# Kernel tuning notes

Measured on AMD Instinct MI355X. Metric: run time of the kernel, lower is better.

The kernel has to match this reference:

```python
import jax, jax.numpy as jnp
import numpy as np

N = 100000
E = 1600000
D_IN = 128
HEADS = 4
C = 16  # hidden // heads
NEG_SLOPE = 0.2


def setup_inputs() -> dict:
    key = jax.random.key(0)
    ks = jax.random.split(key, 8)
    x = jax.random.normal(ks[0], (N, D_IN), dtype=jnp.float32)
    edge_index = jax.random.randint(ks[1], (2, E), 0, N, dtype=jnp.int32)
    s = 1.0 / np.sqrt(D_IN)
    W_l = jax.random.normal(ks[2], (D_IN, HEADS * C), dtype=jnp.float32) * s
    b_l = jnp.zeros((HEADS * C,), dtype=jnp.float32)
    W_r = jax.random.normal(ks[3], (D_IN, HEADS * C), dtype=jnp.float32) * s
    b_r = jnp.zeros((HEADS * C,), dtype=jnp.float32)
    att = jax.random.normal(ks[4], (HEADS, C), dtype=jnp.float32) * (1.0 / np.sqrt(C))
    bias = jnp.zeros((HEADS * C,), dtype=jnp.float32)
    W_head = jax.random.normal(ks[5], (HEADS * C, 1), dtype=jnp.float32) * (1.0 / np.sqrt(HEADS * C))
    b_head = jnp.zeros((1,), dtype=jnp.float32)
    return {"x": x, "edge_index": edge_index, "W_l": W_l, "b_l": b_l,
            "W_r": W_r, "b_r": b_r, "att": att, "bias": bias,
            "W_head": W_head, "b_head": b_head}


def reference(x, edge_index, W_l, b_l, W_r, b_r, att, bias, W_head, b_head):
    # GATv2Conv (PyG semantics, add_self_loops=True, concat=True)
    n = x.shape[0]
    # add self loops
    loops = jnp.arange(n, dtype=edge_index.dtype)
    src = jnp.concatenate([edge_index[0], loops])  # source j
    dst = jnp.concatenate([edge_index[1], loops])  # target i
    # per-node linear projections -> [N, H, C]
    x_l = (x @ W_l + b_l).reshape(n, HEADS, C)
    x_r = (x @ W_r + b_r).reshape(n, HEADS, C)
    # per-edge attention logits: att . LeakyReLU(x_l[j] + x_r[i])
    e = x_l[src] + x_r[dst]                               # [E', H, C]
    e = jnp.where(e >= 0, e, NEG_SLOPE * e)
    logits = jnp.einsum('ehc,hc->eh', e, att)             # [E', H]
    # segment softmax over incoming edges of each target node
    seg_max = jax.ops.segment_max(logits, dst, num_segments=n)  # [N, H]
    expw = jnp.exp(logits - seg_max[dst])
    seg_sum = jax.ops.segment_sum(expw, dst, num_segments=n)
    alpha = expw / seg_sum[dst]                           # [E', H]
    # weighted scatter-aggregate of source messages
    msg = alpha[:, :, None] * x_l[src]                    # [E', H, C]
    out = jax.ops.segment_sum(msg, dst, num_segments=n)   # [N, H, C]
    out = out.reshape(n, HEADS * C) + bias
    # ReLU + Linear head
    h = jax.nn.relu(out)
    return (h @ W_head + b_head).squeeze(-1)              # [N]
```

## Files before the change

### kernel.cpp

```cpp
#include <hip/hip_runtime.h>
#include <hip/hip_bf16.h>
#include <hip/hip_fp16.h>

#define HC 64
#define D_IN 128
#define NEG_SLOPE 0.2f
#define BK 64
#define BCAP2 1536
#define NBIN 2048
#define L2E 1.44269504f

using f32x4 = __attribute__((ext_vector_type(4))) float;
using f16x8 = __attribute__((ext_vector_type(8))) _Float16;
using f16x2 = __attribute__((ext_vector_type(2))) _Float16;

__global__ __launch_bounds__(256, 4) void k_proj(
    const float* __restrict__ x,
    const float* __restrict__ Wl, const float* __restrict__ bl,
    const float* __restrict__ Wr, const float* __restrict__ br,
    __half* __restrict__ xlh, float* __restrict__ xr,
    int* __restrict__ bfill, int N) {
    if (blockIdx.x < 8) {
        const int i = blockIdx.x * 256 + threadIdx.x;
        bfill[i] = i * BCAP2;
    }
    const int t = threadIdx.x;
    const int lane = t & 63;
    const int wave = t >> 6;
    const int m = lane & 15;
    const int q = lane >> 4;

    f16x8 bf[2][4];
    float bfu[2];
#pragma unroll
    for (int cc = 0; cc < 2; ++cc) {
        const int ct = wave * 2 + cc;
        const int ch = (ct & 3) * 16 + m;
        const float* W = (ct < 4) ? Wl : Wr;
        bfu[cc] = (ct < 4) ? bl[ch] : br[ch];
#pragma unroll
        for (int kk = 0; kk < 4; ++kk) {
            const float* wp = W + (size_t)(kk * 32 + q * 8) * 64 + ch;
            f16x8 v;
#pragma unroll
            for (int e = 0; e < 8; ++e)
                v[e] = (_Float16)wp[(size_t)e * 64];
            bf[cc][kk] = v;
        }
    }

    const int ntrip = N >> 5;
    for (int trip = blockIdx.x; trip < ntrip; trip += gridDim.x) {
        const int i0 = trip << 5;
        f16x8 af[2][4];
#pragma unroll
        for (int tt = 0; tt < 2; ++tt) {
            const float* xp = x + (size_t)(i0 + tt * 16 + m) * D_IN + q * 8;
#pragma unroll
            for (int kk = 0; kk < 4; ++kk) {
                const float4 f0 = *(const float4*)(xp + kk * 32);
                const float4 f1 = *(const float4*)(xp + kk * 32 + 4);
                f16x8 v;
                v[0] = (_Float16)f0.x; v[1] = (_Float16)f0.y;
                v[2] = (_Float16)f0.z; v[3] = (_Float16)f0.w;
                v[4] = (_Float16)f1.x; v[5] = (_Float16)f1.y;
                v[6] = (_Float16)f1.z; v[7] = (_Float16)f1.w;
                af[tt][kk] = v;
            }
        }
#pragma unroll
        for (int cc = 0; cc < 2; ++cc) {
            const int ct = wave * 2 + cc;
            f32x4 acc0 = {0.f, 0.f, 0.f, 0.f};
            f32x4 acc1 = {0.f, 0.f, 0.f, 0.f};
#pragma unroll
            for (int kk = 0; kk < 4; ++kk) {
                acc0 = __builtin_amdgcn_mfma_f32_16x16x32_f16(af[0][kk], bf[cc][kk], acc0, 0, 0, 0);
                acc1 = __builtin_amdgcn_mfma_f32_16x16x32_f16(af[1][kk], bf[cc][kk], acc1, 0, 0, 0);
            }
            const float bv = bfu[cc];
            if (ct < 4) {
                const int ch = ct * 16 + m;
#pragma unroll
                for (int r = 0; r < 4; ++r) {
                    xlh[(size_t)(i0 + q * 4 + r) * HC + ch]      = __float2half(acc0[r] + bv);
                    xlh[(size_t)(i0 + 16 + q * 4 + r) * HC + ch] = __float2half(acc1[r] + bv);
                }
            } else {
                const int ch = (ct - 4) * 16 + m;
#pragma unroll
                for (int r = 0; r < 4; ++r) {
                    xr[(size_t)(i0 + q * 4 + r) * HC + ch]      = acc0[r] + bv;
                    xr[(size_t)(i0 + 16 + q * 4 + r) * HC + ch] = acc1[r] + bv;
                }
            }
        }
    }
}

__global__ __launch_bounds__(256) void k_scat1(const int* __restrict__ src,
                                               const int* __restrict__ dst, int E,
                                               int* __restrict__ bfill,
                                               unsigned* __restrict__ coarse) {
    __shared__ int h[NBIN], bl[NBIN], cur[NBIN];
    const int t = threadIdx.x;
    for (int i = t; i < NBIN; i += 256) { h[i] = 0; cur[i] = 0; }
    __syncthreads();
    const int beg = blockIdx.x * 4096;
    int4 d4[4], s4[4];
#pragma unroll
    for (int r = 0; r < 4; ++r) {
        const int idx = beg + 4 * t + r * 1024;
        if (idx < E) {
            d4[r] = *(const int4*)(dst + idx);
            s4[r] = *(const int4*)(src + idx);
        } else { d4[r] = make_int4(-1, -1, -1, -1); }
    }
#pragma unroll
    for (int r = 0; r < 4; ++r) {
        if (d4[r].x >= 0) {
            atomicAdd(&h[d4[r].x >> 6], 1);
            atomicAdd(&h[d4[r].y >> 6], 1);
            atomicAdd(&h[d4[r].z >> 6], 1);
            atomicAdd(&h[d4[r].w >> 6], 1);
        }
    }
    __syncthreads();
    for (int i = t; i < NBIN; i += 256)
        bl[i] = h[i] ? atomicAdd(&bfill[i], h[i]) : 0;
    __syncthreads();
#pragma unroll
    for (int r = 0; r < 4; ++r) {
        if (d4[r].x >= 0) {
            const int dd[4] = {d4[r].x, d4[r].y, d4[r].z, d4[r].w};
            const int ss[4] = {s4[r].x, s4[r].y, s4[r].z, s4[r].w};
#pragma unroll
            for (int j = 0; j < 4; ++j) {
                const int bin = dd[j] >> 6;
                const int pos = atomicAdd(&cur[bin], 1);
                coarse[bl[bin] + pos] = ((unsigned)ss[j] << 6) | (unsigned)(dd[j] & 63);
            }
        }
    }
}

__device__ __forceinline__ float redpair(float v) {
    int a = __builtin_amdgcn_update_dpp(0, __float_as_int(v), 0xB1, 0xF, 0xF, true);
    return v + __int_as_float(a);
}

__global__ __launch_bounds__(256) void k_aggs(
    const __half* __restrict__ xlh, const float* __restrict__ xr,
    const float* __restrict__ att, const float* __restrict__ bias,
    const float* __restrict__ Wh, const float* __restrict__ bh,
    const int* __restrict__ bfill, const unsigned* __restrict__ coarse,
    float* __restrict__ out, int N) {
    __shared__ int s_src[BCAP2];
    __shared__ int s_cnt[BK], s_off[BK], s_cur[BK], s_scan[BK];
    const int t = threadIdx.x;
    const int b = blockIdx.x;
    const int eb = b * BCAP2;
    const int ee = bfill[b];
    if (t < BK) { s_cnt[t] = 0; s_cur[t] = 0; }
    __syncthreads();
    unsigned er[6]; int nr = 0;
#pragma unroll
    for (int r = 0; r < 6; ++r) {
        const int idx = eb + t + r * 256;
        if (idx < ee) er[nr++] = coarse[idx];
    }
    for (int k = 0; k < nr; ++k) atomicAdd(&s_cnt[er[k] & 63], 1);
    __syncthreads();
    if (t < BK) s_scan[t] = s_cnt[t];
    __syncthreads();
    for (int o = 1; o < BK; o <<= 1) {
        int v = (t < BK && t >= o) ? s_scan[t - o] : 0;
        __syncthreads();
        if (t < BK) s_scan[t] += v;
        __syncthreads();
    }
    if (t < BK) s_off[t] = s_scan[t] - s_cnt[t];
    __syncthreads();
    for (int k = 0; k < nr; ++k) {
        const int bin = er[k] & 63;
        const int pos = atomicAdd(&s_cur[bin], 1);
        s_src[s_off[bin] + pos] = (int)(er[k] >> 6);
    }
    __syncthreads();

    const int wave = t >> 6;
    const int lane = t & 63;
    const int sub  = lane & 7;
    const int slot = lane >> 3;
    const _Float16* xlhp = (const _Float16*)xlh;

    const float4 atA = *(const float4*)(att + 8 * sub);
    const float4 atB = *(const float4*)(att + 8 * sub + 4);
    f16x2 at[4];
    at[0][0] = (_Float16)(atA.x * L2E); at[0][1] = (_Float16)(atA.y * L2E);
    at[1][0] = (_Float16)(atA.z * L2E); at[1][1] = (_Float16)(atA.w * L2E);
    at[2][0] = (_Float16)(atB.x * L2E); at[2][1] = (_Float16)(atB.y * L2E);
    at[3][0] = (_Float16)(atB.z * L2E); at[3][1] = (_Float16)(atB.w * L2E);
    const f16x2 c02 = {(_Float16)NEG_SLOPE, (_Float16)NEG_SLOPE};
    const float4 biA = *(const float4*)(bias + 8 * sub);
    const float4 biB = *(const float4*)(bias + 8 * sub + 4);
    const float4 whA = *(const float4*)(Wh + 8 * sub);
    const float4 whB = *(const float4*)(Wh + 8 * sub + 4);
    const float bhv = bh[0];

    for (int k16 = 0; k16 < 16; ++k16) {
        const int nl = wave + 4 * k16;
        const int i = (b << 6) + nl;
        if (i >= N) continue;
        const int beg = s_off[nl];
        const int cnt = s_cnt[nl];

        const float4 xrA = *(const float4*)(xr + ((size_t)i << 6) + 8 * sub);
        const float4 xrB = *(const float4*)(xr + ((size_t)i << 6) + 8 * sub + 4);
        f16x2 xri[4];
        xri[0][0] = (_Float16)xrA.x; xri[0][1] = (_Float16)xrA.y;
        xri[1][0] = (_Float16)xrA.z; xri[1][1] = (_Float16)xrA.w;
        xri[2][0] = (_Float16)xrB.x; xri[2][1] = (_Float16)xrB.y;
        xri[3][0] = (_Float16)xrB.z; xri[3][1] = (_Float16)xrB.w;
        const uint4 xliraw = *(const uint4*)(xlhp + ((size_t)i << 6) + 8 * sub);
        f16x2 xli[4];
        xli[0] = __builtin_bit_cast(f16x2, xliraw.x);
        xli[1] = __builtin_bit_cast(f16x2, xliraw.y);
        xli[2] = __builtin_bit_cast(f16x2, xliraw.z);
        xli[3] = __builtin_bit_cast(f16x2, xliraw.w);

        float t0 = 0.f;
#pragma unroll
        for (int c = 0; c < 4; ++c) {
            f16x2 w = xli[c] + xri[c];
            w = __builtin_elementwise_max(w, w * c02);
            t0 = __builtin_amdgcn_fdot2(at[c], w, t0, false);
        }
        t0 = redpair(t0);
        const float pe0 = (slot == 0) ? exp2f(t0) : 0.f;
        float s = pe0;
        float a[8];
#pragma unroll
        for (int c = 0; c < 4; ++c) {
            a[2 * c]     = pe0 * (float)xli[c][0];
            a[2 * c + 1] = pe0 * (float)xli[c][1];
        }

        int p = 0;
#define EDGE_GROUP(JEXPR, PRED)                                              \
    {                                                                        \
        const int jj = (JEXPR);                                              \
        const uint4 raw = *(const uint4*)(xlhp + ((size_t)jj << 6) + 8 * sub);\
        f16x2 xv[4];                                                         \
        xv[0] = __builtin_bit_cast(f16x2, raw.x);                            \
        xv[1] = __builtin_bit_cast(f16x2, raw.y);                            \
        xv[2] = __builtin_bit_cast(f16x2, raw.z);                            \
        xv[3] = __builtin_bit_cast(f16x2, raw.w);                            \
        float tt = 0.f;                                                      \
        _Pragma("unroll")                                                    \
        for (int c = 0; c < 4; ++c) {                                        \
            f16x2 w = xv[c] + xri[c];                                        \
            w = __builtin_elementwise_max(w, w * c02);                       \
            tt = __builtin_amdgcn_fdot2(at[c], w, tt, false);                \
        }                                                                    \
        tt = redpair(tt);                                                    \
        const float pe = (PRED) ? exp2f(tt) : 0.f;                           \
        s += pe;                                                             \
        _Pragma("unroll")                                                    \
        for (int c = 0; c < 4; ++c) {                                        \
            a[2 * c]     = fmaf(pe, (float)xv[c][0], a[2 * c]);              \
            a[2 * c + 1] = fmaf(pe, (float)xv[c][1], a[2 * c + 1]);          \
        }                                                                    \
    }
        for (; p + 16 <= cnt; p += 16) {
            const int j0 = s_src[beg + p + slot];
            const int j1 = s_src[beg + p + 8 + slot];
            EDGE_GROUP(j0, true)
            EDGE_GROUP(j1, true)
        }
        if (p + 8 <= cnt) {
            const int j0 = s_src[beg + p + slot];
            EDGE_GROUP(j0, true)
            p += 8;
        }
        const int rem = cnt - p;
        if (rem > 0) {
            const int idx = p + slot;
            const int j0 = s_src[beg + ((idx < cnt) ? idx : (cnt - 1))];
            EDGE_GROUP(j0, slot < rem)
        }
#undef EDGE_GROUP

        s += __shfl_xor(s, 8);  s += __shfl_xor(s, 16);  s += __shfl_xor(s, 32);
#pragma unroll
        for (int c = 0; c < 8; ++c) {
            a[c] += __shfl_xor(a[c], 8);
            a[c] += __shfl_xor(a[c], 16);
            a[c] += __shfl_xor(a[c], 32);
        }
        const float inv = 1.f / s;
        float y = fmaxf(a[0] * inv + biA.x, 0.f) * whA.x
                + fmaxf(a[1] * inv + biA.y, 0.f) * whA.y
                + fmaxf(a[2] * inv + biA.z, 0.f) * whA.z
                + fmaxf(a[3] * inv + biA.w, 0.f) * whA.w
                + fmaxf(a[4] * inv + biB.x, 0.f) * whB.x
                + fmaxf(a[5] * inv + biB.y, 0.f) * whB.y
                + fmaxf(a[6] * inv + biB.z, 0.f) * whB.z
                + fmaxf(a[7] * inv + biB.w, 0.f) * whB.w;
        y += __shfl_xor(y, 1);
        y += __shfl_xor(y, 2);
        y += __shfl_xor(y, 4);
        if (lane == 0) out[i] = y + bhv;
    }
}

extern "C" void kernel_launch(void* const* d_in, const int* in_sizes, int n_in,
                              void* d_out, int out_size, void* d_ws, size_t ws_size,
                              hipStream_t stream) {
    const float* x   = (const float*)d_in[0];
    const int*   ei  = (const int*)d_in[1];
    const float* Wl  = (const float*)d_in[2];
    const float* bl  = (const float*)d_in[3];
    const float* Wr  = (const float*)d_in[4];
    const float* br  = (const float*)d_in[5];
    const float* att = (const float*)d_in[6];
    const float* bias= (const float*)d_in[7];
    const float* Wh  = (const float*)d_in[8];
    const float* bh  = (const float*)d_in[9];
    float* out = (float*)d_out;

    const int N = in_sizes[0] / D_IN;
    const int E = in_sizes[1] / 2;
    const int* src = ei;
    const int* dst = ei + E;
    const int nbkt = (N + BK - 1) / BK;

    auto align = [](size_t v) { return (v + 255) & ~(size_t)255; };
    char* ws = (char*)d_ws;
    size_t off = 0;
    __half* xlh     = (__half*)(ws + off);   off = align(off + (size_t)N * HC * 2);
    float* xr       = (float*)(ws + off);    off = align(off + (size_t)N * HC * 4);
    int*   bfill    = (int*)(ws + off);      off = align(off + NBIN * 4);
    unsigned* coarse= (unsigned*)(ws + off); off = align(off + (size_t)NBIN * BCAP2 * 4);
    (void)ws_size;

    k_proj<<<1024, 256, 0, stream>>>(x, Wl, bl, Wr, br, xlh, xr, bfill, N);

    k_scat1<<<(E + 4095) / 4096, 256, 0, stream>>>(src, dst, E, bfill, coarse);

    k_aggs<<<nbkt, 256, 0, stream>>>(xlh, xr, att, bias, Wh, bh,
                                     bfill, coarse, out, N);
}
```

Measured before the change: 220.3 us.

## Merge projection and edge-binning kernels; interleave two nodes per wave in aggregation

Projection and the edge scatter/binning now run as one kernel, with a block-index split, so the two independent phases overlap on the GPU. The bfill initialisation moves to a small separate kernel. The aggregation kernel now processes two destination nodes per wave at once and issues their gathers together, raising memory-level parallelism for the random xl loads. The cost is 24KB of shared memory on the projection blocks, which may reduce their occupancy, plus higher register pressure in the aggregation loop.

Result: slower. 227.8 us (+3.4%).

```diff
diff --git a/kernel.cpp b/kernel.cpp
--- a/kernel.cpp
+++ b/kernel.cpp
@@ -14,17 +14,66 @@
 using f16x8 = __attribute__((ext_vector_type(8))) _Float16;
 using f16x2 = __attribute__((ext_vector_type(2))) _Float16;
 
-__global__ __launch_bounds__(256, 4) void k_proj(
+__global__ void k_iota(int* __restrict__ p, int n) {
+    int i = blockIdx.x * blockDim.x + threadIdx.x;
+    if (i < n) p[i] = i * BCAP2;
+}
+
+__global__ __launch_bounds__(256, 4) void k_projscat(
     const float* __restrict__ x,
     const float* __restrict__ Wl, const float* __restrict__ bl,
     const float* __restrict__ Wr, const float* __restrict__ br,
     __half* __restrict__ xlh, float* __restrict__ xr,
-    int* __restrict__ bfill, int N) {
-    if (blockIdx.x < 8) {
-        const int i = blockIdx.x * 256 + threadIdx.x;
-        bfill[i] = i * BCAP2;
-    }
+    const int* __restrict__ src, const int* __restrict__ dst, int E,
+    int* __restrict__ bfill, unsigned* __restrict__ coarse, int N) {
+    __shared__ int h[NBIN], sbl[NBIN], cur[NBIN];
     const int t = threadIdx.x;
+    const int nscat = (E + 4095) >> 12;
+
+    if ((int)blockIdx.x < nscat) {
+        for (int i = t; i < NBIN; i += 256) { h[i] = 0; cur[i] = 0; }
+        __syncthreads();
+        const int beg = blockIdx.x * 4096;
+        int4 d4[4], s4[4];
+#pragma unroll
+        for (int r = 0; r < 4; ++r) {
+            const int idx = beg + 4 * t + r * 1024;
+            if (idx < E) {
+                d4[r] = *(const int4*)(dst + idx);
+                s4[r] = *(const int4*)(src + idx);
+            } else { d4[r] = make_int4(-1, -1, -1, -1); }
+        }
+#pragma unroll
+        for (int r = 0; r < 4; ++r) {
+            if (d4[r].x >= 0) {
+                atomicAdd(&h[d4[r].x >> 6], 1);
+                atomicAdd(&h[d4[r].y >> 6], 1);
+                atomicAdd(&h[d4[r].z >> 6], 1);
+                atomicAdd(&h[d4[r].w >> 6], 1);
+            }
+        }
+        __syncthreads();
+        for (int i = t; i < NBIN; i += 256)
+            sbl[i] = h[i] ? atomicAdd(&bfill[i], h[i]) : 0;
+        __syncthreads();
+#pragma unroll
+        for (int r = 0; r < 4; ++r) {
+            if (d4[r].x >= 0) {
+                const int dd[4] = {d4[r].x, d4[r].y, d4[r].z, d4[r].w};
+                const int ss[4] = {s4[r].x, s4[r].y, s4[r].z, s4[r].w};
+#pragma unroll
+                for (int j = 0; j < 4; ++j) {
+                    const int bin = dd[j] >> 6;
+                    const int pos = atomicAdd(&cur[bin], 1);
+                    coarse[sbl[bin] + pos] = ((unsigned)ss[j] << 6) | (unsigned)(dd[j] & 63);
+                }
+            }
+        }
+        return;
+    }
+
+    const int pb  = blockIdx.x - nscat;
+    const int npb = gridDim.x - nscat;
     const int lane = t & 63;
     const int wave = t >> 6;
     const int m = lane & 15;
@@ -50,7 +99,7 @@
     }
 
     const int ntrip = N >> 5;
-    for (int trip = blockIdx.x; trip < ntrip; trip += gridDim.x) {
+    for (int trip = pb; trip < ntrip; trip += npb) {
         const int i0 = trip << 5;
         f16x8 af[2][4];
 #pragma unroll
@@ -93,52 +142,6 @@
                     xr[(size_t)(i0 + q * 4 + r) * HC + ch]      = acc0[r] + bv;
                     xr[(size_t)(i0 + 16 + q * 4 + r) * HC + ch] = acc1[r] + bv;
                 }
-            }
-        }
-    }
-}
-
-__global__ __launch_bounds__(256) void k_scat1(const int* __restrict__ src,
-                                               const int* __restrict__ dst, int E,
-                                               int* __restrict__ bfill,
-                                               unsigned* __restrict__ coarse) {
-    __shared__ int h[NBIN], bl[NBIN], cur[NBIN];
-    const int t = threadIdx.x;
-    for (int i = t; i < NBIN; i += 256) { h[i] = 0; cur[i] = 0; }
-    __syncthreads();
-    const int beg = blockIdx.x * 4096;
-    int4 d4[4], s4[4];
-#pragma unroll
-    for (int r = 0; r < 4; ++r) {
-        const int idx = beg + 4 * t + r * 1024;
-        if (idx < E) {
-            d4[r] = *(const int4*)(dst + idx);
-            s4[r] = *(const int4*)(src + idx);
-        } else { d4[r] = make_int4(-1, -1, -1, -1); }
-    }
-#pragma unroll
-    for (int r = 0; r < 4; ++r) {
-        if (d4[r].x >= 0) {
-            atomicAdd(&h[d4[r].x >> 6], 1);
-            atomicAdd(&h[d4[r].y >> 6], 1);
-            atomicAdd(&h[d4[r].z >> 6], 1);
-            atomicAdd(&h[d4[r].w >> 6], 1);
-        }
-    }
-    __syncthreads();
-    for (int i = t; i < NBIN; i += 256)
-        bl[i] = h[i] ? atomicAdd(&bfill[i], h[i]) : 0;
-    __syncthreads();
-#pragma unroll
-    for (int r = 0; r < 4; ++r) {
-        if (d4[r].x >= 0) {
-            const int dd[4] = {d4[r].x, d4[r].y, d4[r].z, d4[r].w};
-            const int ss[4] = {s4[r].x, s4[r].y, s4[r].z, s4[r].w};
-#pragma unroll
-            for (int j = 0; j < 4; ++j) {
-                const int bin = dd[j] >> 6;
-                const int pos = atomicAdd(&cur[bin], 1);
-                coarse[bl[bin] + pos] = ((unsigned)ss[j] << 6) | (unsigned)(dd[j] & 63);
             }
         }
     }
@@ -208,110 +211,205 @@
     const float4 whB = *(const float4*)(Wh + 8 * sub + 4);
     const float bhv = bh[0];
 
-    for (int k16 = 0; k16 < 16; ++k16) {
-        const int nl = wave + 4 * k16;
-        const int i = (b << 6) + nl;
-        if (i >= N) continue;
-        const int beg = s_off[nl];
-        const int cnt = s_cnt[nl];
-
-        const float4 xrA = *(const float4*)(xr + ((size_t)i << 6) + 8 * sub);
-        const float4 xrB = *(const float4*)(xr + ((size_t)i << 6) + 8 * sub + 4);
-        f16x2 xri[4];
-        xri[0][0] = (_Float16)xrA.x; xri[0][1] = (_Float16)xrA.y;
-        xri[1][0] = (_Float16)xrA.z; xri[1][1] = (_Float16)xrA.w;
-        xri[2][0] = (_Float16)xrB.x; xri[2][1] = (_Float16)xrB.y;
-        xri[3][0] = (_Float16)xrB.z; xri[3][1] = (_Float16)xrB.w;
-        const uint4 xliraw = *(const uint4*)(xlhp + ((size_t)i << 6) + 8 * sub);
-        f16x2 xli[4];
-        xli[0] = __builtin_bit_cast(f16x2, xliraw.x);
-        xli[1] = __builtin_bit_cast(f16x2, xliraw.y);
-        xli[2] = __builtin_bit_cast(f16x2, xliraw.z);
-        xli[3] = __builtin_bit_cast(f16x2, xliraw.w);
-
-        float t0 = 0.f;
-#pragma unroll
-        for (int c = 0; c < 4; ++c) {
-            f16x2 w = xli[c] + xri[c];
-            w = __builtin_elementwise_max(w, w * c02);
-            t0 = __builtin_amdgcn_fdot2(at[c], w, t0, false);
-        }
-        t0 = redpair(t0);
-        const float pe0 = (slot == 0) ? exp2f(t0) : 0.f;
-        float s = pe0;
-        float a[8];
-#pragma unroll
-        for (int c = 0; c < 4; ++c) {
-            a[2 * c]     = pe0 * (float)xli[c][0];
-            a[2 * c + 1] = pe0 * (float)xli[c][1];
-        }
-
-        int p = 0;
-#define EDGE_GROUP(JEXPR, PRED)                                              \
+#define EG_LOAD(RAW, J)                                                      \
+    const uint4 RAW = *(const uint4*)(xlhp + ((size_t)(J) << 6) + 8 * sub);
+
+#define EG_COMP(RAW, XRI, S, A, PRED)                                        \
     {                                                                        \
-        const int jj = (JEXPR);                                              \
-        const uint4 raw = *(const uint4*)(xlhp + ((size_t)jj << 6) + 8 * sub);\
         f16x2 xv[4];                                                         \
-        xv[0] = __builtin_bit_cast(f16x2, raw.x);                            \
-        xv[1] = __builtin_bit_cast(f16x2, raw.y);                            \
-        xv[2] = __builtin_bit_cast(f16x2, raw.z);                            \
-        xv[3] = __builtin_bit_cast(f16x2, raw.w);                            \
+        xv[0] = __builtin_bit_cast(f16x2, RAW.x);                            \
+        xv[1] = __builtin_bit_cast(f16x2, RAW.y);                            \
+        xv[2] = __builtin_bit_cast(f16x2, RAW.z);                            \
+        xv[3] = __builtin_bit_cast(f16x2, RAW.w);                            \
         float tt = 0.f;                                                      \
         _Pragma("unroll")                                                    \
         for (int c = 0; c < 4; ++c) {                                        \
-            f16x2 w = xv[c] + xri[c];                                        \
+            f16x2 w = xv[c] + XRI[c];                                        \
             w = __builtin_elementwise_max(w, w * c02);                       \
             tt = __builtin_amdgcn_fdot2(at[c], w, tt, false);                \
         }                                                                    \
         tt = redpair(tt);                                                    \
         const float pe = (PRED) ? exp2f(tt) : 0.f;                           \
-        s += pe;                                                             \
+        S += pe;                                                             \
         _Pragma("unroll")                                                    \
         for (int c = 0; c < 4; ++c) {                                        \
-            a[2 * c]     = fmaf(pe, (float)xv[c][0], a[2 * c]);              \
-            a[2 * c + 1] = fmaf(pe, (float)xv[c][1], a[2 * c + 1]);          \
+            A[2 * c]     = fmaf(pe, (float)xv[c][0], A[2 * c]);              \
+            A[2 * c + 1] = fmaf(pe, (float)xv[c][1], A[2 * c + 1]);          \
         }                                                                    \
     }
-        for (; p + 16 <= cnt; p += 16) {
-            const int j0 = s_src[beg + p + slot];
-            const int j1 = s_src[beg + p + 8 + slot];
-            EDGE_GROUP(j0, true)
-            EDGE_GROUP(j1, true)
-        }
-        if (p + 8 <= cnt) {
-            const int j0 = s_src[beg + p + slot];
-            EDGE_GROUP(j0, true)
-            p += 8;
-        }
-        const int rem = cnt - p;
-        if (rem > 0) {
-            const int idx = p + slot;
-            const int j0 = s_src[beg + ((idx < cnt) ? idx : (cnt - 1))];
-            EDGE_GROUP(j0, slot < rem)
-        }
-#undef EDGE_GROUP
-
-        s += __shfl_xor(s, 8);  s += __shfl_xor(s, 16);  s += __shfl_xor(s, 32);
+
+#define SELF_INIT(XLI, XRI, S, A)                                            \
+    {                                                                        \
+        float t0 = 0.f;                                                      \
+        _Pragma("unroll")                                                    \
+        for (int c = 0; c < 4; ++c) {                                        \
+            f16x2 w = XLI[c] + XRI[c];                                       \
+            w = __builtin_elementwise_max(w, w * c02);                       \
+            t0 = __builtin_amdgcn_fdot2(at[c], w, t0, false);                \
+        }                                                                    \
+        t0 = redpair(t0);                                                    \
+        const float pe0 = (slot == 0) ? exp2f(t0) : 0.f;                     \
+        S = pe0;                                                             \
+        _Pragma("unroll")                                                    \
+        for (int c = 0; c < 4; ++c) {                                        \
+            A[2 * c]     = pe0 * (float)XLI[c][0];                           \
+            A[2 * c + 1] = pe0 * (float)XLI[c][1];                           \
+        }                                                                    \
+    }
+
+    for (int k8 = 0; k8 < 8; ++k8) {
+        const int nl0 = wave + 8 * k8;
+        const int nl1 = nl0 + 4;
+        const int i0n = (b << 6) + nl0;
+        const int i1n = (b << 6) + nl1;
+        const bool v0 = i0n < N;
+        const bool v1 = i1n < N;
+        const int is0 = v0 ? i0n : 0;
+        const int is1 = v1 ? i1n : 0;
+        const int beg0 = s_off[nl0];
+        const int cnt0 = v0 ? s_cnt[nl0] : 0;
+        const int beg1 = s_off[nl1];
+        const int cnt1 = v1 ? s_cnt[nl1] : 0;
+
+        const float4 xr0a = *(const float4*)(xr + ((size_t)is0 << 6) + 8 * sub);
+        const float4 xr0b = *(const float4*)(xr + ((size_t)is0 << 6) + 8 * sub + 4);
+        const uint4  xl0r = *(const uint4*)(xlhp + ((size_t)is0 << 6) + 8 * sub);
+        const float4 xr1a = *(const float4*)(xr + ((size_t)is1 << 6) + 8 * sub);
+        const float4 xr1b = *(const float4*)(xr + ((size_t)is1 << 6) + 8 * sub + 4);
+        const uint4  xl1r = *(const uint4*)(xlhp + ((size_t)is1 << 6) + 8 * sub);
+
+        f16x2 xri0[4], xli0[4], xri1[4], xli1[4];
+        xri0[0][0] = (_Float16)xr0a.x; xri0[0][1] = (_Float16)xr0a.y;
+        xri0[1][0] = (_Float16)xr0a.z; xri0[1][1] = (_Float16)xr0a.w;
+        xri0[2][0] = (_Float16)xr0b.x; xri0[2][1] = (_Float16)xr0b.y;
+        xri0[3][0] = (_Float16)xr0b.z; xri0[3][1] = (_Float16)xr0b.w;
+        xri1[0][0] = (_Float16)xr1a.x; xri1[0][1] = (_Float16)xr1a.y;
+        xri1[1][0] = (_Float16)xr1a.z; xri1[1][1] = (_Float16)xr1a.w;
+        xri1[2][0] = (_Float16)xr1b.x; xri1[2][1] = (_Float16)xr1b.y;
+        xri1[3][0] = (_Float16)xr1b.z; xri1[3][1] = (_Float16)xr1b.w;
+        xli0[0] = __builtin_bit_cast(f16x2, xl0r.x);
+        xli0[1] = __builtin_bit_cast(f16x2, xl0r.y);
+        xli0[2] = __builtin_bit_cast(f16x2, xl0r.z);
+        xli0[3] = __builtin_bit_cast(f16x2, xl0r.w);
+        xli1[0] = __builtin_bit_cast(f16x2, xl1r.x);
+        xli1[1] = __builtin_bit_cast(f16x2, xl1r.y);
+        xli1[2] = __builtin_bit_cast(f16x2, xl1r.z);
+        xli1[3] = __builtin_bit_cast(f16x2, xl1r.w);
+
+        float s0, s1, a0[8], a1[8];
+        SELF_INIT(xli0, xri0, s0, a0)
+        SELF_INIT(xli1, xri1, s1, a1)
+
+        int p0 = 0, p1 = 0;
+        while (p0 + 16 <= cnt0 && p1 + 16 <= cnt1) {
+            const int j00 = s_src[beg0 + p0 + slot];
+            const int j01 = s_src[beg0 + p0 + 8 + slot];
+            const int j10 = s_src[beg1 + p1 + slot];
+            const int j11 = s_src[beg1 + p1 + 8 + slot];
+            EG_LOAD(r00, j00)
+            EG_LOAD(r01, j01)
+            EG_LOAD(r10, j10)
+            EG_LOAD(r11, j11)
+            EG_COMP(r00, xri0, s0, a0, true)
+            EG_COMP(r01, xri0, s0, a0, true)
+            EG_COMP(r10, xri1, s1, a1, true)
+            EG_COMP(r11, xri1, s1, a1, true)
+            p0 += 16; p1 += 16;
+        }
+        while (p0 + 8 <= cnt0 && p1 + 8 <= cnt1) {
+            const int j00 = s_src[beg0 + p0 + slot];
+            const int j10 = s_src[beg1 + p1 + slot];
+            EG_LOAD(r00, j00)
+            EG_LOAD(r10, j10)
+            EG_COMP(r00, xri0, s0, a0, true)
+            EG_COMP(r10, xri1, s1, a1, true)
+            p0 += 8; p1 += 8;
+        }
+        for (; p0 + 16 <= cnt0; p0 += 16) {
+            const int ja = s_src[beg0 + p0 + slot];
+            const int jb = s_src[beg0 + p0 + 8 + slot];
+            EG_LOAD(ra, ja)
+            EG_LOAD(rb, jb)
+            EG_COMP(ra, xri0, s0, a0, true)
+            EG_COMP(rb, xri0, s0, a0, true)
+        }
+        if (p0 + 8 <= cnt0) {
+            const int ja = s_src[beg0 + p0 + slot];
+            EG_LOAD(ra, ja)
+            EG_COMP(ra, xri0, s0, a0, true)
+            p0 += 8;
+        }
+        {
+            const int rem = cnt0 - p0;
+            if (rem > 0) {
+                const int idx = p0 + slot;
+                const int ja = s_src[beg0 + ((idx < cnt0) ? idx : (cnt0 - 1))];
+                EG_LOAD(ra, ja)
+                EG_COMP(ra, xri0, s0, a0, slot < rem)
+            }
+        }
+        for (; p1 + 16 <= cnt1; p1 += 16) {
+            const int ja = s_src[beg1 + p1 + slot];
+            const int jb = s_src[beg1 + p1 + 8 + slot];
+            EG_LOAD(ra, ja)
+            EG_LOAD(rb, jb)
+            EG_COMP(ra, xri1, s1, a1, true)
+            EG_COMP(rb, xri1, s1, a1, true)
+        }
+        if (p1 + 8 <= cnt1) {
+            const int ja = s_src[beg1 + p1 + slot];
+            EG_LOAD(ra, ja)
+            EG_COMP(ra, xri1, s1, a1, true)
+            p1 += 8;
+        }
+        {
+            const int rem = cnt1 - p1;
+            if (rem > 0) {
+                const int idx = p1 + slot;
+                const int ja = s_src[beg1 + ((idx < cnt1) ? idx : (cnt1 - 1))];
+                EG_LOAD(ra, ja)
+                EG_COMP(ra, xri1, s1, a1, slot < rem)
+            }
+        }
+
+        s0 += __shfl_xor(s0, 8);  s1 += __shfl_xor(s1, 8);
+        s0 += __shfl_xor(s0, 16); s1 += __shfl_xor(s1, 16);
+        s0 += __shfl_xor(s0, 32); s1 += __shfl_xor(s1, 32);
 #pragma unroll
         for (int c = 0; c < 8; ++c) {
-            a[c] += __shfl_xor(a[c], 8);
-            a[c] += __shfl_xor(a[c], 16);
-            a[c] += __shfl_xor(a[c], 32);
-        }
-        const float inv = 1.f / s;
-        float y = fmaxf(a[0] * inv + biA.x, 0.f) * whA.x
-                + fmaxf(a[1] * inv + biA.y, 0.f) * whA.y
-                + fmaxf(a[2] * inv + biA.z, 0.f) * whA.z
-                + fmaxf(a[3] * inv + biA.w, 0.f) * whA.w
-                + fmaxf(a[4] * inv + biB.x, 0.f) * whB.x
-                + fmaxf(a[5] * inv + biB.y, 0.f) * whB.y
-                + fmaxf(a[6] * inv + biB.z, 0.f) * whB.z
-                + fmaxf(a[7] * inv + biB.w, 0.f) * whB.w;
-        y += __shfl_xor(y, 1);
-        y += __shfl_xor(y, 2);
-        y += __shfl_xor(y, 4);
-        if (lane == 0) out[i] = y + bhv;
-    }
+            a0[c] += __shfl_xor(a0[c], 8);  a1[c] += __shfl_xor(a1[c], 8);
+            a0[c] += __shfl_xor(a0[c], 16); a1[c] += __shfl_xor(a1[c], 16);
+            a0[c] += __shfl_xor(a0[c], 32); a1[c] += __shfl_xor(a1[c], 32);
+        }
+        const float inv0 = 1.f / s0;
+        const float inv1 = 1.f / s1;
+        float y0 = fmaxf(a0[0] * inv0 + biA.x, 0.f) * whA.x
+                 + fmaxf(a0[1] * inv0 + biA.y, 0.f) * whA.y
+                 + fmaxf(a0[2] * inv0 + biA.z, 0.f) * whA.z
+                 + fmaxf(a0[3] * inv0 + biA.w, 0.f) * whA.w
+                 + fmaxf(a0[4] * inv0 + biB.x, 0.f) * whB.x
+                 + fmaxf(a0[5] * inv0 + biB.y, 0.f) * whB.y
+                 + fmaxf(a0[6] * inv0 + biB.z, 0.f) * whB.z
+                 + fmaxf(a0[7] * inv0 + biB.w, 0.f) * whB.w;
+        float y1 = fmaxf(a1[0] * inv1 + biA.x, 0.f) * whA.x
+                 + fmaxf(a1[1] * inv1 + biA.y, 0.f) * whA.y
+                 + fmaxf(a1[2] * inv1 + biA.z, 0.f) * whA.z
+                 + fmaxf(a1[3] * inv1 + biA.w, 0.f) * whA.w
+                 + fmaxf(a1[4] * inv1 + biB.x, 0.f) * whB.x
+                 + fmaxf(a1[5] * inv1 + biB.y, 0.f) * whB.y
+                 + fmaxf(a1[6] * inv1 + biB.z, 0.f) * whB.z
+                 + fmaxf(a1[7] * inv1 + biB.w, 0.f) * whB.w;
+        y0 += __shfl_xor(y0, 1);  y1 += __shfl_xor(y1, 1);
+        y0 += __shfl_xor(y0, 2);  y1 += __shfl_xor(y1, 2);
+        y0 += __shfl_xor(y0, 4);  y1 += __shfl_xor(y1, 4);
+        if (lane == 0) {
+            if (v0) out[i0n] = y0 + bhv;
+            if (v1) out[i1n] = y1 + bhv;
+        }
+    }
+#undef EG_LOAD
+#undef EG_COMP
+#undef SELF_INIT
 }
 
 extern "C" void kernel_launch(void* const* d_in, const int* in_sizes, int n_in,
@@ -334,6 +432,7 @@
     const int* src = ei;
     const int* dst = ei + E;
     const int nbkt = (N + BK - 1) / BK;
+    const int nscat = (E + 4095) / 4096;
 
     auto align = [](size_t v) { return (v + 255) & ~(size_t)255; };
     char* ws = (char*)d_ws;
@@ -344,9 +443,10 @@
     unsigned* coarse= (unsigned*)(ws + off); off = align(off + (size_t)NBIN * BCAP2 * 4);
     (void)ws_size;
 
-    k_proj<<<1024, 256, 0, stream>>>(x, Wl, bl, Wr, br, xlh, xr, bfill, N);
-
-    k_scat1<<<(E + 4095) / 4096, 256, 0, stream>>>(src, dst, E, bfill, coarse);
+    k_iota<<<8, 256, 0, stream>>>(bfill, NBIN);
+
+    k_projscat<<<nscat + 1024, 256, 0, stream>>>(x, Wl, bl, Wr, br, xlh, xr,
+                                                 src, dst, E, bfill, coarse, N);
 
     k_aggs<<<nbkt, 256, 0, stream>>>(xlh, xr, att, bias, Wh, bh,
                                      bfill, coarse, out, N);
```
